# Optimization experiments

Hardware: AMD Instinct MI355X
Metric: run time of the kernel (lower is better)

Reference implementation:

```python
import jax, jax.numpy as jnp
import numpy as np

N = 10000        # nodes
F_IN = 128       # node features (data.num_node_features)
OUT = 16         # out_channels
H = 32           # attention heads
C1 = 4 * OUT     # hidden per-head dim (4*out_channels)
E = 80000        # directed edges
EPS = 1e-5       # BatchNorm eps
NEG = 0.2        # GATConv LeakyReLU negative_slope


def _gat(x, src, dst, W, a_s, a_d, b, n, C):
    # PyG GATConv, shared lin, concat=False (mean over heads)
    h = (x @ W).reshape(n, H, C)                    # [n,H,C]
    e_src = jnp.sum(h * a_s, -1)                    # [n,H] (alpha from x_j)
    e_dst = jnp.sum(h * a_d, -1)                    # [n,H] (alpha from x_i)
    e = jax.nn.leaky_relu(e_src[src] + e_dst[dst], NEG)     # [E',H]
    m = jax.ops.segment_max(e, dst, num_segments=n)         # segment softmax
    p = jnp.exp(e - m[dst])
    z = jax.ops.segment_sum(p, dst, num_segments=n)
    alpha = p / z[dst]
    out = jax.ops.segment_sum(alpha[:, :, None] * h[src], dst, num_segments=n)
    return out.mean(1) + b                          # mean over heads + bias


def _bn(x, g, b, m, v):  # eval-mode BatchNorm1d (running stats)
    return (x - m) * g / jnp.sqrt(v + EPS) + b


def setup_inputs():
    k = jax.random.split(jax.random.key(0), 40)
    rn = lambda i, s, sc=0.1: jax.random.normal(k[i], s, jnp.float32) * sc
    d = {"x": jax.random.normal(k[0], (N, F_IN), jnp.float32),
         "edge_index": jax.random.randint(k[1], (2, E), 0, N, jnp.int32)}
    # 4 GATConv layers
    d.update(W1=rn(2, (F_IN, H * C1)), as1=rn(3, (H, C1)), ad1=rn(4, (H, C1)), b1=rn(5, (C1,)))
    d.update(W2=rn(6, (C1, H * OUT)), as2=rn(7, (H, OUT)), ad2=rn(8, (H, OUT)), b2=rn(9, (OUT,)))
    d.update(W3=rn(10, (F_IN, H * C1)), as3=rn(11, (H, C1)), ad3=rn(12, (H, C1)), b3=rn(13, (C1,)))
    d.update(W4=rn(14, (C1, H * OUT)), as4=rn(15, (H, OUT)), ad4=rn(16, (H, OUT)), b4=rn(17, (OUT,)))
    # ResidualNetwork(1 block): 1x1 Conv1d over L=1 == matmul
    d.update(rwa=rn(18, (F_IN, OUT)), rba=rn(19, (OUT,)),
             bn1g=jnp.ones(OUT), bn1b=jnp.zeros(OUT), bn1m=rn(20, (OUT,)), bn1v=jnp.abs(rn(21, (OUT,))) + 1.0,
             rwb=rn(22, (OUT, OUT)), rbb=rn(23, (OUT,)),
             bn2g=jnp.ones(OUT), bn2b=jnp.zeros(OUT), bn2m=rn(24, (OUT,)), bn2v=jnp.abs(rn(25, (OUT,))) + 1.0,
             wsc=rn(26, (F_IN, OUT)), bsc=rn(27, (OUT,)),
             bnsg=jnp.ones(OUT), bnsb=jnp.zeros(OUT), bnsm=rn(28, (OUT,)), bnsv=jnp.abs(rn(29, (OUT,))) + 1.0,
             wfc=rn(30, (OUT, OUT)), bfc=rn(31, (OUT,)))
    return d


def reference(x, edge_index, W1, as1, ad1, b1, W2, as2, ad2, b2,
              W3, as3, ad3, b3, W4, as4, ad4, b4,
              rwa, rba, bn1g, bn1b, bn1m, bn1v, rwb, rbb, bn2g, bn2b, bn2m, bn2v,
              wsc, bsc, bnsg, bnsb, bnsm, bnsv, wfc, bfc):
    n = x.shape[0]
    loops = jnp.arange(n, dtype=edge_index.dtype)  # add_self_loops=True
    s2t_src = jnp.concatenate([edge_index[0], loops])  # flow source_to_target
    s2t_dst = jnp.concatenate([edge_index[1], loops])
    t2s_src = jnp.concatenate([edge_index[1], loops])  # flow target_to_source
    t2s_dst = jnp.concatenate([edge_index[0], loops])
    # dropout in original is unassigned (no-op); eval mode assumed
    x_s = jax.nn.elu(_gat(x, s2t_src, s2t_dst, W1, as1, ad1, b1, n, C1))
    x_in = jax.nn.elu(_gat(x_s, s2t_src, s2t_dst, W2, as2, ad2, b2, n, OUT))
    x_t = jax.nn.elu(_gat(x, t2s_src, t2s_dst, W3, as3, ad3, b3, n, C1))
    x_out = jax.nn.elu(_gat(x_t, t2s_src, t2s_dst, W4, as4, ad4, b4, n, OUT))
    # ResidualNetwork: block + identity avg-pool (L=1) + fc
    h = jax.nn.relu(_bn(x @ rwa + rba, bn1g, bn1b, bn1m, bn1v))
    h = _bn(h @ rwb + rbb, bn2g, bn2b, bn2m, bn2v)
    sc = _bn(x @ wsc + bsc, bnsg, bnsb, bnsm, bnsv)
    x_self = jax.nn.relu(h + sc) @ wfc + bfc
    return (x_in, x_out, x_self)
```

## Files before the change

kernel.cpp:

```cpp
#include <hip/hip_runtime.h>
#include <stdint.h>

__device__ __forceinline__ float bf2f(unsigned short u) {
  union { unsigned int i; float f; } v; v.i = ((unsigned int)u) << 16; return v.f;
}
__device__ __forceinline__ unsigned short f2bf(float f) {
  union { float f; unsigned int i; } v; v.f = f;
  unsigned int i = v.i;
  unsigned int r = (i + 0x7fffu + ((i >> 16) & 1u)) >> 16;
  return (unsigned short)r;
}

typedef __bf16 bf16x8 __attribute__((ext_vector_type(8)));
typedef float f32x4 __attribute__((ext_vector_type(4)));
union ABfrag { int4 i4; bf16x8 v; };

#if __has_builtin(__builtin_amdgcn_cvt_pk_fp8_f32) && __has_builtin(__builtin_amdgcn_cvt_pk_f32_fp8)
#define HW_FP8 1
#else
#define HW_FP8 0
#endif

__device__ __forceinline__ unsigned char f2fp8_sw(float f) {
  union { float f; unsigned int u; } v; v.f = f;
  unsigned int s = (v.u >> 24) & 0x80;
  float a = fabsf(f);
  if (a >= 448.f) return (unsigned char)(s | 0x7E);
  v.f = a;
  int ex = (int)(v.u >> 23);
  unsigned int man = v.u & 0x7FFFFFu;
  if (ex >= 121) {
    unsigned int val = ((unsigned int)(ex - 120) << 3) | (man >> 20);
    unsigned int rem = man & 0xFFFFFu;
    if (rem > 0x80000u || (rem == 0x80000u && (val & 1))) val++;
    if (val > 0x7E) val = 0x7E;
    return (unsigned char)(s | val);
  }
  int q = (int)(a * 512.f + 0.5f);
  if (q > 8) q = 8;
  return (unsigned char)(s | (unsigned int)q);
}
__device__ __forceinline__ float fp8dec_sw(unsigned char c) {
  unsigned int e = (c >> 3) & 15u, m = c & 7u;
  float v;
  if (e) { union { unsigned int u; float f; } x; x.u = ((e + 120) << 23) | (m << 20); v = x.f; }
  else v = (float)m * 0.001953125f;
  return (c & 0x80) ? -v : v;
}
__device__ __forceinline__ unsigned char f2fp8(float f) {
#if HW_FP8
  int v = __builtin_amdgcn_cvt_pk_fp8_f32(f, f, 0, false);
  return (unsigned char)(v & 0xFF);
#else
  return f2fp8_sw(f);
#endif
}
__device__ __forceinline__ void dec16(int4 g, float o[16]) {
#if HW_FP8
  { auto p = __builtin_amdgcn_cvt_pk_f32_fp8(g.x, false); o[0]=p[0]; o[1]=p[1]; }
  { auto p = __builtin_amdgcn_cvt_pk_f32_fp8(g.x, true ); o[2]=p[0]; o[3]=p[1]; }
  { auto p = __builtin_amdgcn_cvt_pk_f32_fp8(g.y, false); o[4]=p[0]; o[5]=p[1]; }
  { auto p = __builtin_amdgcn_cvt_pk_f32_fp8(g.y, true ); o[6]=p[0]; o[7]=p[1]; }
  { auto p = __builtin_amdgcn_cvt_pk_f32_fp8(g.z, false); o[8]=p[0]; o[9]=p[1]; }
  { auto p = __builtin_amdgcn_cvt_pk_f32_fp8(g.z, true ); o[10]=p[0]; o[11]=p[1]; }
  { auto p = __builtin_amdgcn_cvt_pk_f32_fp8(g.w, false); o[12]=p[0]; o[13]=p[1]; }
  { auto p = __builtin_amdgcn_cvt_pk_f32_fp8(g.w, true ); o[14]=p[0]; o[15]=p[1]; }
#else
  unsigned int w[4] = {(unsigned)g.x, (unsigned)g.y, (unsigned)g.z, (unsigned)g.w};
#pragma unroll
  for (int d = 0; d < 4; ++d)
#pragma unroll
    for (int b = 0; b < 4; ++b) o[d*4+b] = fp8dec_sw((unsigned char)((w[d] >> (b*8)) & 0xFF));
#endif
}

__device__ __forceinline__ float lrelu_clamp(float e) {
  e = (e > 0.f) ? e : 0.2f * e;
  return fminf(e, 80.f);
}

__global__ __launch_bounds__(256) void k_detect(const unsigned int* __restrict__ x, int* flag) {
  __shared__ int cnt;
  if (threadIdx.x == 0) cnt = 0;
  __syncthreads();
  int c = 0;
  for (int i = threadIdx.x; i < 1024; i += 256) {
    unsigned int lo = x[i] & 0xFFFFu;
    int ex = (int)((lo >> 7) & 0xFF);
    if (ex >= 100 && ex <= 140) c++;
  }
  atomicAdd(&cnt, c);
  __syncthreads();
  if (threadIdx.x == 0) flag[0] = (cnt > 600) ? 1 : 0;
}

struct PrepDesc {
  const void* csrc[32]; float* cdst[32]; int cn[32];
  const void* x; float* xc; unsigned short* xp;
  const void* W1; const void* W2; const void* W3; const void* W4;
  unsigned short* P1; unsigned short* P2; unsigned short* P3; unsigned short* P4;
  int* degAB;
  int nxb, xtotal, ctotal, ndeg2;
};
__global__ __launch_bounds__(256) void k_prep(PrepDesc d, const int* __restrict__ flag) {
  int isbf = *flag;
  int b = blockIdx.x;
  if (b < d.nxb) {
    int i = b * 256 + threadIdx.x;
    if (i < d.xtotal) {
      float v = isbf ? bf2f(((const unsigned short*)d.x)[i]) : ((const float*)d.x)[i];
      d.xc[i] = v;
      int row = i >> 7, c = i & 127;
      int tm = row >> 4, mr = row & 15;
      int s = c >> 5, quad = (c >> 3) & 3, j = c & 7;
      size_t idx = (((size_t)tm * 4 + s) * 64 + quad * 16 + mr) * 8 + j;
      d.xp[idx] = f2bf(v);
    }
    return;
  }
  b -= d.nxb;
  if (b < 288) {
    int u = b * 256 + threadIdx.x;
    const void* W; unsigned short* P; int K, N, lu;
    if (u < 32768)      { W = d.W1; P = d.P1; K = 128; N = 2048; lu = u; }
    else if (u < 36864) { W = d.W2; P = d.P2; K = 64;  N = 512;  lu = u - 32768; }
    else if (u < 69632) { W = d.W3; P = d.P3; K = 128; N = 2048; lu = u - 36864; }
    else                { W = d.W4; P = d.P4; K = 64;  N = 512;  lu = u - 69632; }
    int ksteps = K >> 5;
    int g = lu / (ksteps * 64);
    int rem = lu - g * (ksteps * 64);
    int s = rem >> 6, lane = rem & 63;
    int mr = lane & 15, quad = lane >> 4;
    int col = g * 16 + mr;
    int kbase = s * 32 + quad * 8;
#pragma unroll
    for (int j = 0; j < 8; ++j) {
      size_t src = (size_t)(kbase + j) * N + col;
      float v = isbf ? bf2f(((const unsigned short*)W)[src]) : ((const float*)W)[src];
      P[(size_t)lu * 8 + j] = f2bf(v);
    }
    return;
  }
  b -= 288;
  if (b < 4) {
    for (int idx = b * 256 + threadIdx.x; idx < d.ctotal; idx += 4 * 256) {
      int t = 0, off = idx;
      while (off >= d.cn[t]) { off -= d.cn[t]; ++t; }
      float v = isbf ? bf2f(((const unsigned short*)d.csrc[t])[off])
                     : ((const float*)d.csrc[t])[off];
      d.cdst[t][off] = v;
    }
    return;
  }
  b -= 4;
  for (int idx = b * 256 + threadIdx.x; idx < d.ndeg2; idx += 8 * 256) d.degAB[idx] = 0;
}

__global__ __launch_bounds__(256) void k_deg_count(const int* __restrict__ ei, int* degA, int* degB, int E) {
  int e = blockIdx.x * 256 + threadIdx.x;
  if (e < E) { atomicAdd(&degA[ei[E + e]], 1); atomicAdd(&degB[ei[e]], 1); }
}
__global__ __launch_bounds__(1024) void k_exscan2(const int* __restrict__ degA, const int* __restrict__ degB,
                                                  int* __restrict__ rowA, int* __restrict__ rowB,
                                                  int* __restrict__ colA, int* __restrict__ colB,
                                                  int* __restrict__ curA, int* __restrict__ curB, int n) {
  const int* deg = (blockIdx.x == 0) ? degA : degB;
  int* row = (blockIdx.x == 0) ? rowA : rowB;
  int* colx = (blockIdx.x == 0) ? colA : colB;
  int* curx = (blockIdx.x == 0) ? curA : curB;
  __shared__ int wsum[16], wbase[16];
  __shared__ int carry;
  if (threadIdx.x == 0) carry = 0;
  __syncthreads();
  int lane = threadIdx.x & 63, w = threadIdx.x >> 6;
  int chunks = (n + 1023) >> 10;
  for (int ch = 0; ch < chunks; ++ch) {
    int i = (ch << 10) + threadIdx.x;
    int v = (i < n) ? deg[i] : 0;
    int sc = v;
#pragma unroll
    for (int o = 1; o < 64; o <<= 1) { int t = __shfl_up(sc, o); if (lane >= o) sc += t; }
    if (lane == 63) wsum[w] = sc;
    __syncthreads();
    if (threadIdx.x < 16) {
      int v2 = wsum[threadIdx.x], s2 = v2;
#pragma unroll
      for (int o = 1; o < 16; o <<= 1) { int t = __shfl_up(s2, o); if (lane >= o) s2 += t; }
      wbase[threadIdx.x] = s2 - v2;
      if (threadIdx.x == 15) wsum[15] = s2;
    }
    __syncthreads();
    if (i < n) {
      int rv = carry + wbase[w] + (sc - v) + i;
      row[i] = rv;
      colx[rv] = i;
      curx[i] = rv + 1;
    }
    __syncthreads();
    if (threadIdx.x == 0) carry += wsum[15];
    __syncthreads();
  }
  if (threadIdx.x == 0) row[n] = carry + n;
}
__global__ __launch_bounds__(256) void k_scatter(const int* __restrict__ ei, int* colA, int* colB,
                                                 int* curA, int* curB, int E) {
  int e = blockIdx.x * 256 + threadIdx.x;
  if (e < E) {
    int s = ei[e], d = ei[E + e];
    colA[atomicAdd(&curA[d], 1)] = s;
    colB[atomicAdd(&curB[s], 1)] = d;
  }
}

union SMem {
  unsigned char tile[4][16][64];
  struct { float xs[16][128]; float ha[16][16]; float tt[16][16]; } res;
};

template<int CH, int KSTEPS>
__device__ __forceinline__ void mm_es_body(int vblk,
    const unsigned short* __restrict__ Ap, const unsigned short* __restrict__ Bp,
    unsigned char* __restrict__ C, const float* __restrict__ a_s, const float* __restrict__ a_d,
    float* __restrict__ es, float* __restrict__ ed, int N, SMem* sm) {
  int wid = threadIdx.x >> 6;
  int wg = vblk * 4 + wid;
  int ntiles = N >> 6;
  int tm = wg / ntiles, tn = wg % ntiles;
  int lane = threadIdx.x & 63;
  int mr = lane & 15, quad = lane >> 4;
  const unsigned short* ap = Ap + ((size_t)tm * KSTEPS) * 512 + lane * 8;
  const unsigned short* bp = Bp + ((size_t)tn * 4 * KSTEPS) * 512 + lane * 8;
  f32x4 acc[4];
#pragma unroll
  for (int i = 0; i < 4; i++) acc[i] = (f32x4){0.f, 0.f, 0.f, 0.f};
#pragma unroll
  for (int s = 0; s < KSTEPS; ++s) {
    ABfrag a; a.i4 = *(const int4*)(ap + s * 512);
#pragma unroll
    for (int nt = 0; nt < 4; ++nt) {
      ABfrag b; b.i4 = *(const int4*)(bp + (size_t)(nt * KSTEPS + s) * 512);
      acc[nt] = __builtin_amdgcn_mfma_f32_16x16x32_bf16(a.v, b.v, acc[nt], 0, 0, 0);
    }
  }
#pragma unroll
  for (int nt = 0; nt < 4; ++nt)
#pragma unroll
    for (int r = 0; r < 4; ++r)
      sm->tile[wid][quad * 4 + r][nt * 16 + mr] = f2fp8(acc[nt][r]);
  __syncthreads();
  {
    int r16 = lane >> 2, seg = lane & 3;
    int4 val = *(const int4*)&sm->tile[wid][r16][seg * 16];
    *(int4*)(C + (size_t)(tm * 16 + r16) * N + tn * 64 + seg * 16) = val;
  }
  if (CH == 64) {
    float pes[4] = {0.f,0.f,0.f,0.f}, ped[4] = {0.f,0.f,0.f,0.f};
    const float* asr = a_s + tn * 64;
    const float* adr = a_d + tn * 64;
#pragma unroll
    for (int nt = 0; nt < 4; ++nt) {
      float ws = asr[nt * 16 + mr], wd = adr[nt * 16 + mr];
#pragma unroll
      for (int r = 0; r < 4; ++r) { pes[r] += acc[nt][r] * ws; ped[r] += acc[nt][r] * wd; }
    }
#pragma unroll
    for (int m = 1; m < 16; m <<= 1)
#pragma unroll
      for (int r = 0; r < 4; ++r) {
        pes[r] += __shfl_xor(pes[r], m);
        ped[r] += __shfl_xor(ped[r], m);
      }
    if (mr == 0) {
#pragma unroll
      for (int r = 0; r < 4; ++r) {
        int row = tm * 16 + quad * 4 + r;
        es[row * 32 + tn] = pes[r];
        ed[row * 32 + tn] = ped[r];
      }
    }
  } else {
    float pes[4][4], ped[4][4];
#pragma unroll
    for (int nt = 0; nt < 4; ++nt) {
      float ws = a_s[(tn * 4 + nt) * 16 + mr];
      float wd = a_d[(tn * 4 + nt) * 16 + mr];
#pragma unroll
      for (int r = 0; r < 4; ++r) { pes[nt][r] = acc[nt][r] * ws; ped[nt][r] = acc[nt][r] * wd; }
    }
#pragma unroll
    for (int m = 1; m < 16; m <<= 1)
#pragma unroll
      for (int nt = 0; nt < 4; ++nt)
#pragma unroll
        for (int r = 0; r < 4; ++r) {
          pes[nt][r] += __shfl_xor(pes[nt][r], m);
          ped[nt][r] += __shfl_xor(ped[nt][r], m);
        }
    if (mr == 0) {
#pragma unroll
      for (int nt = 0; nt < 4; ++nt)
#pragma unroll
        for (int r = 0; r < 4; ++r) {
          int row = tm * 16 + quad * 4 + r;
          es[row * 32 + tn * 4 + nt] = pes[nt][r];
          ed[row * 32 + tn * 4 + nt] = ped[nt][r];
        }
    }
  }
}

struct MM13Desc {
  const unsigned short* Ap;
  const unsigned short* B1; const unsigned short* B3;
  unsigned char* C1; unsigned char* C3;
  const float* as1; const float* ad1; const float* as3; const float* ad3;
  float* es1; float* ed1; float* es3; float* ed3;
  int mmblks;
  const float* xc;
  const float* rp[20];
  void* outbase; size_t eoff; int n;
  const int* flag;
};
__global__ __launch_bounds__(256) void k_mm13res(MM13Desc d) {
  __shared__ SMem sm;
  int b = blockIdx.x;
  if (b < d.mmblks) {
    mm_es_body<64,4>(b, d.Ap, d.B1, d.C1, d.as1, d.ad1, d.es1, d.ed1, 2048, &sm);
    return;
  }
  b -= d.mmblks;
  if (b < d.mmblks) {
    mm_es_body<64,4>(b, d.Ap, d.B3, d.C3, d.as3, d.ad3, d.es3, d.ed3, 2048, &sm);
    return;
  }
  b -= d.mmblks;
  int nodebase = b * 16;
  for (int t = threadIdx.x; t < 16 * 128; t += 256)
    sm.res.xs[t >> 7][t & 127] = d.xc[(size_t)(nodebase + (t >> 7)) * 128 + (t & 127)];
  __syncthreads();
  int ni = threadIdx.x >> 4, c = threadIdx.x & 15;
  const float* rwa = d.rp[0]; const float* rba = d.rp[1];
  const float* bn1g = d.rp[2]; const float* bn1b = d.rp[3];
  const float* bn1m = d.rp[4]; const float* bn1v = d.rp[5];
  const float* rwb = d.rp[6]; const float* rbb = d.rp[7];
  const float* bn2g = d.rp[8]; const float* bn2b = d.rp[9];
  const float* bn2m = d.rp[10]; const float* bn2v = d.rp[11];
  const float* wsc = d.rp[12]; const float* bsc = d.rp[13];
  const float* bnsg = d.rp[14]; const float* bnsb = d.rp[15];
  const float* bnsm = d.rp[16]; const float* bnsv = d.rp[17];
  const float* wfc = d.rp[18]; const float* bfc = d.rp[19];
  float ya = 0.f, ysc = 0.f;
  for (int k = 0; k < 128; ++k) {
    float xv = sm.res.xs[ni][k];
    ya  += xv * rwa[k * 16 + c];
    ysc += xv * wsc[k * 16 + c];
  }
  ya += rba[c]; ysc += bsc[c];
  float s1 = bn1g[c] * rsqrtf(bn1v[c] + 1e-5f);
  ya = (ya - bn1m[c]) * s1 + bn1b[c];
  ya = fmaxf(ya, 0.f);
  float ss = bnsg[c] * rsqrtf(bnsv[c] + 1e-5f);
  ysc = (ysc - bnsm[c]) * ss + bnsb[c];
  sm.res.ha[ni][c] = ya;
  __syncthreads();
  float h2 = rbb[c];
  for (int k = 0; k < 16; ++k) h2 += sm.res.ha[ni][k] * rwb[k * 16 + c];
  float s2 = bn2g[c] * rsqrtf(bn2v[c] + 1e-5f);
  h2 = (h2 - bn2m[c]) * s2 + bn2b[c];
  sm.res.tt[ni][c] = fmaxf(h2 + ysc, 0.f);
  __syncthreads();
  float o = bfc[c];
  for (int k = 0; k < 16; ++k) o += sm.res.tt[ni][k] * wfc[k * 16 + c];
  size_t oo = d.eoff + (size_t)(nodebase + ni) * 16 + c;
  if (*d.flag) ((unsigned short*)d.outbase)[oo] = f2bf(o);
  else         ((float*)d.outbase)[oo] = o;
}

__global__ __launch_bounds__(256) void k_g64(const unsigned char* __restrict__ h1,
                                             const unsigned char* __restrict__ h3,
                                             const float* __restrict__ es1, const float* __restrict__ ed1,
                                             const float* __restrict__ es3, const float* __restrict__ ed3,
                                             const int* __restrict__ rowA, const int* __restrict__ colA,
                                             const int* __restrict__ rowB, const int* __restrict__ colB,
                                             const float* __restrict__ b1, const float* __restrict__ b3,
                                             unsigned short* __restrict__ xsp, unsigned short* __restrict__ xtp,
                                             int n, int gb) {
  int b = blockIdx.x;
  const unsigned char* h; const float *es, *ed, *bias; const int *rowp, *col; unsigned short* outp;
  if (b < gb) { h = h1; es = es1; ed = ed1; rowp = rowA; col = colA; bias = b1; outp = xsp; }
  else { b -= gb; h = h3; es = es3; ed = ed3; rowp = rowB; col = colB; bias = b3; outp = xtp; }
  int wid = threadIdx.x >> 6, lane = threadIdx.x & 63;
  int i = b * 4 + wid;
  if (i >= n) return;
  int hd0 = lane >> 2, hd1 = 16 + hd0;
  float e0 = ed[i * 32 + hd0];
  float e1 = ed[i * 32 + hd1];
  int beg = rowp[i], end = rowp[i + 1];
  int deg = end - beg;
  int colv = (lane < deg) ? col[beg + lane] : 0;
  float acc0[16], acc1[16];
#pragma unroll
  for (int k = 0; k < 16; ++k) { acc0[k] = 0.f; acc1[k] = 0.f; }
  float Z0 = 0.f, Z1 = 0.f;
  for (int j = 0; j < deg; ++j) {
    int s = (j < 64) ? __shfl(colv, j) : col[beg + j];
    const int4* hp = (const int4*)(h + (size_t)s * 2048);
    int4 g0 = hp[lane];
    int4 g1 = hp[64 + lane];
    float q0 = __expf(lrelu_clamp(es[s * 32 + hd0] + e0));
    float q1 = __expf(lrelu_clamp(es[s * 32 + hd1] + e1));
    Z0 += q0; Z1 += q1;
    float d0[16], d1[16];
    dec16(g0, d0); dec16(g1, d1);
#pragma unroll
    for (int k = 0; k < 16; ++k) { acc0[k] += q0 * d0[k]; acc1[k] += q1 * d1[k]; }
  }
  float zi0 = 1.0f / Z0, zi1 = 1.0f / Z1;
  float v[16];
#pragma unroll
  for (int k = 0; k < 16; ++k) v[k] = acc0[k] * zi0 + acc1[k] * zi1;
#pragma unroll
  for (int m = 4; m < 64; m <<= 1)
#pragma unroll
    for (int k = 0; k < 16; ++k) v[k] += __shfl_xor(v[k], m);
  if (lane < 4) {
    int tm = i >> 4, mr = i & 15;
    unsigned short ob[16];
#pragma unroll
    for (int k = 0; k < 16; ++k) {
      float t = v[k] * (1.f / 32.f) + bias[lane * 16 + k];
      t = (t > 0.f) ? t : (__expf(t) - 1.f);
      ob[k] = f2bf(t);
    }
    int s0 = lane >> 1;
#pragma unroll
    for (int g2 = 0; g2 < 2; ++g2) {
      size_t idx = (((size_t)tm * 2 + s0) * 64 + ((lane & 1) * 2 + g2) * 16 + mr) * 8;
      *(int4*)(outp + idx) = *(const int4*)(ob + g2 * 8);
    }
  }
}

__global__ __launch_bounds__(256) void k_mm24(const unsigned short* __restrict__ xsp,
                                              const unsigned short* __restrict__ xtp,
                                              const unsigned short* __restrict__ W2p,
                                              const unsigned short* __restrict__ W4p,
                                              unsigned char* __restrict__ h2, unsigned char* __restrict__ h4,
                                              const float* __restrict__ as2, const float* __restrict__ ad2,
                                              const float* __restrict__ as4, const float* __restrict__ ad4,
                                              float* __restrict__ es2, float* __restrict__ ed2,
                                              float* __restrict__ es4, float* __restrict__ ed4,
                                              int mmblks) {
  __shared__ SMem sm;
  int b = blockIdx.x;
  if (b < mmblks)
    mm_es_body<16,2>(b, xsp, W2p, h2, as2, ad2, es2, ed2, 512, &sm);
  else
    mm_es_body<16,2>(b - mmblks, xtp, W4p, h4, as4, ad4, es4, ed4, 512, &sm);
}

__global__ __launch_bounds__(256) void k_g16(const unsigned char* __restrict__ h2,
                                             const unsigned char* __restrict__ h4,
                                             const float* __restrict__ es2, const float* __restrict__ ed2,
                                             const float* __restrict__ es4, const float* __restrict__ ed4,
                                             const int* __restrict__ rowA, const int* __restrict__ colA,
                                             const int* __restrict__ rowB, const int* __restrict__ colB,
                                             const float* __restrict__ b2, const float* __restrict__ b4,
                                             void* __restrict__ outbase, int n, int gb,
                                             const int* __restrict__ flag) {
  int b = blockIdx.x;
  const unsigned char* h; const float *es, *ed, *bias; const int *rowp, *col; size_t eoff;
  if (b < gb) { h = h2; es = es2; ed = ed2; rowp = rowA; col = colA; bias = b2; eoff = 0; }
  else { b -= gb; h = h4; es = es4; ed = ed4; rowp = rowB; col = colB; bias = b4; eoff = (size_t)n * 16; }
  int wid = threadIdx.x >> 6, lane = threadIdx.x & 63;
  int i = b * 4 + wid;
  if (i >= n) return;
  int hh = lane & 31, j2 = lane >> 5;
  float ev = ed[i * 32 + hh];
  int beg = rowp[i], end = rowp[i + 1];
  int deg = end - beg;
  int colv = (lane < deg) ? col[beg + lane] : 0;
  float acc[16];
#pragma unroll
  for (int k = 0; k < 16; ++k) acc[k] = 0.f;
  float Z = 0.f;
  for (int j = j2; j < deg; j += 2) {
    int s = (j < 64) ? __shfl(colv, j) : col[beg + j];
    int4 g = ((const int4*)(h + (size_t)s * 512))[hh];
    float q = __expf(lrelu_clamp(es[s * 32 + hh] + ev));
    Z += q;
    float d[16];
    dec16(g, d);
#pragma unroll
    for (int k = 0; k < 16; ++k) acc[k] += q * d[k];
  }
  Z += __shfl_xor(Z, 32);
  float zi = 1.0f / Z;
  float v[16];
#pragma unroll
  for (int k = 0; k < 16; ++k) v[k] = acc[k] * zi;
#pragma unroll
  for (int m = 1; m < 64; m <<= 1)
#pragma unroll
    for (int k = 0; k < 16; ++k) v[k] += __shfl_xor(v[k], m);
  if (lane == 0) {
    int isbf = *flag;
    if (isbf) {
      unsigned short ob[16];
#pragma unroll
      for (int k = 0; k < 16; ++k) {
        float t = v[k] * (1.f / 32.f) + bias[k];
        t = (t > 0.f) ? t : (__expf(t) - 1.f);
        ob[k] = f2bf(t);
      }
      unsigned short* o = (unsigned short*)outbase + eoff + (size_t)i * 16;
      *(int4*)o = *(const int4*)ob;
      *(int4*)(o + 8) = *(const int4*)(ob + 8);
    } else {
      float* o = (float*)outbase + eoff + (size_t)i * 16;
#pragma unroll
      for (int k = 0; k < 16; ++k) {
        float t = v[k] * (1.f / 32.f) + bias[k];
        t = (t > 0.f) ? t : (__expf(t) - 1.f);
        o[k] = t;
      }
    }
  }
}

extern "C" void kernel_launch(void* const* d_in, const int* in_sizes, int n_in,
                              void* d_out, int out_size, void* d_ws, size_t ws_size,
                              hipStream_t stream) {
  const int n = in_sizes[0] / 128;
  const int E = in_sizes[1] / 2;
  const int* ei = (const int*)d_in[1];

  char* wsp = (char*)d_ws; size_t off = 0;
  auto alloc = [&](size_t bytes) -> void* {
    void* p = wsp + off; off = (off + bytes + 255) & ~(size_t)255; return p;
  };
  int* flag = (int*)alloc(4);
  float* xc = (float*)alloc((size_t)n * 128 * 4);
  unsigned short* xp = (unsigned short*)alloc((size_t)n * 128 * 2);
  unsigned short* W1p = (unsigned short*)alloc((size_t)2048 * 128 * 2);
  unsigned short* W2p = (unsigned short*)alloc((size_t)512 * 64 * 2);
  unsigned short* W3p = (unsigned short*)alloc((size_t)2048 * 128 * 2);
  unsigned short* W4p = (unsigned short*)alloc((size_t)512 * 64 * 2);
  unsigned char* h1 = (unsigned char*)alloc((size_t)n * 2048);
  unsigned char* h3 = (unsigned char*)alloc((size_t)n * 2048);
  unsigned char* h2 = (unsigned char*)alloc((size_t)n * 512);
  unsigned char* h4 = (unsigned char*)alloc((size_t)n * 512);
  float* es1 = (float*)alloc((size_t)n * 32 * 4);
  float* ed1 = (float*)alloc((size_t)n * 32 * 4);
  float* es3 = (float*)alloc((size_t)n * 32 * 4);
  float* ed3 = (float*)alloc((size_t)n * 32 * 4);
  float* es2 = (float*)alloc((size_t)n * 32 * 4);
  float* ed2 = (float*)alloc((size_t)n * 32 * 4);
  float* es4 = (float*)alloc((size_t)n * 32 * 4);
  float* ed4 = (float*)alloc((size_t)n * 32 * 4);
  unsigned short* xsp = (unsigned short*)alloc((size_t)n * 64 * 2);
  unsigned short* xtp = (unsigned short*)alloc((size_t)n * 64 * 2);
  int* rowA = (int*)alloc((size_t)(n + 1) * 4);
  int* rowB = (int*)alloc((size_t)(n + 1) * 4);
  int* colA = (int*)alloc((size_t)(E + n) * 4);
  int* colB = (int*)alloc((size_t)(E + n) * 4);
  int* degAB = (int*)alloc((size_t)2 * n * 4);
  int* degA = degAB, * degB = degAB + n;
  int* curA = (int*)alloc((size_t)n * 4);
  int* curB = (int*)alloc((size_t)n * 4);

  static const int cidx[32] = {3,4,5, 7,8,9, 11,12,13, 15,16,17,
                               18,19,20,21,22,23,24,25,26,27,28,29,
                               30,31,32,33,34,35,36,37};
  PrepDesc pd;
  float* canon[38] = {nullptr};
  pd.ctotal = 0;
  for (int t = 0; t < 32; ++t) {
    int ii = cidx[t];
    canon[ii] = (float*)alloc((size_t)in_sizes[ii] * 4);
    pd.csrc[t] = d_in[ii];
    pd.cdst[t] = canon[ii];
    pd.cn[t] = in_sizes[ii];
    pd.ctotal += in_sizes[ii];
  }
  pd.x = d_in[0]; pd.xc = xc; pd.xp = xp;
  pd.W1 = d_in[2]; pd.W2 = d_in[6]; pd.W3 = d_in[10]; pd.W4 = d_in[14];
  pd.P1 = W1p; pd.P2 = W2p; pd.P3 = W3p; pd.P4 = W4p;
  pd.degAB = degAB;
  pd.nxb = (n * 128 + 255) / 256;
  pd.xtotal = n * 128;
  pd.ndeg2 = 2 * n;
  (void)ws_size; (void)n_in; (void)out_size;

  k_detect<<<1, 256, 0, stream>>>((const unsigned int*)d_in[0], flag);
  k_prep<<<pd.nxb + 288 + 4 + 8, 256, 0, stream>>>(pd, flag);

  k_deg_count<<<(E + 255) / 256, 256, 0, stream>>>(ei, degA, degB, E);
  k_exscan2<<<2, 1024, 0, stream>>>(degA, degB, rowA, rowB, colA, colB, curA, curB, n);
  k_scatter<<<(E + 255) / 256, 256, 0, stream>>>(ei, colA, colB, curA, curB, E);

  const int mt = n / 16;
  const int mmblks64 = mt * 32 / 4;
  const int mmblks16 = mt * 8 / 4;
  const int gb = (n + 3) / 4;

  MM13Desc md;
  md.Ap = xp; md.B1 = W1p; md.B3 = W3p; md.C1 = h1; md.C3 = h3;
  md.as1 = canon[3]; md.ad1 = canon[4]; md.as3 = canon[11]; md.ad3 = canon[12];
  md.es1 = es1; md.ed1 = ed1; md.es3 = es3; md.ed3 = ed3;
  md.mmblks = mmblks64;
  md.xc = xc;
  for (int t = 0; t < 20; ++t) md.rp[t] = canon[18 + t];
  md.outbase = d_out; md.eoff = (size_t)2 * n * 16; md.n = n; md.flag = flag;
  k_mm13res<<<2 * mmblks64 + n / 16, 256, 0, stream>>>(md);

  k_g64<<<2 * gb, 256, 0, stream>>>(h1, h3, es1, ed1, es3, ed3,
                                    rowA, colA, rowB, colB,
                                    canon[5], canon[13], xsp, xtp, n, gb);
  k_mm24<<<2 * mmblks16, 256, 0, stream>>>(xsp, xtp, W2p, W4p, h2, h4,
                                           canon[7], canon[8], canon[15], canon[16],
                                           es2, ed2, es4, ed4, mmblks16);
  k_g16<<<2 * gb, 256, 0, stream>>>(h2, h4, es2, ed2, es4, ed4,
                                    rowA, colA, rowB, colB,
                                    canon[9], canon[17], d_out, n, gb, flag);
}
```

Before: 323.8 us.

## Fold dtype detection and degree counting into prep kernel; parallelize CSR scan

Removes the separate detect and degree-count launches. Every prep block now recomputes the bf16/fp32 detection itself, and the edge degree atomics run as extra blocks of k_prep, with the degree buffers zeroed by a memset beforehand. The exclusive scan becomes a two-pass chunked scan, one wave per 1024-element chunk, replacing the serial loop over chunks with block-wide syncs. This saves launches and scan serialization, at the cost of each prep block redundantly reading 4KB of x and adding a memset call.

```diff
diff --git a/kernel.cpp b/kernel.cpp
--- a/kernel.cpp
+++ b/kernel.cpp
@@ -79,40 +79,39 @@
   return fminf(e, 80.f);
 }
 
-__global__ __launch_bounds__(256) void k_detect(const unsigned int* __restrict__ x, int* flag) {
-  __shared__ int cnt;
-  if (threadIdx.x == 0) cnt = 0;
-  __syncthreads();
-  int c = 0;
-  for (int i = threadIdx.x; i < 1024; i += 256) {
-    unsigned int lo = x[i] & 0xFFFFu;
-    int ex = (int)((lo >> 7) & 0xFF);
-    if (ex >= 100 && ex <= 140) c++;
-  }
-  atomicAdd(&cnt, c);
-  __syncthreads();
-  if (threadIdx.x == 0) flag[0] = (cnt > 600) ? 1 : 0;
-}
-
 struct PrepDesc {
   const void* csrc[32]; float* cdst[32]; int cn[32];
   const void* x; float* xc; unsigned short* xp;
   const void* W1; const void* W2; const void* W3; const void* W4;
   unsigned short* P1; unsigned short* P2; unsigned short* P3; unsigned short* P4;
-  int* degAB;
-  int nxb, xtotal, ctotal, ndeg2;
+  const int* ei; int* degA; int* degB; int E;
+  int* flagout;
+  int nxb, xtotal, ctotal, ndgb;
 };
-__global__ __launch_bounds__(256) void k_prep(PrepDesc d, const int* __restrict__ flag) {
-  int isbf = *flag;
+__global__ __launch_bounds__(256) void k_prep(PrepDesc d) {
+  int c = 0;
+  for (int i = threadIdx.x; i < 1024; i += 256) {
+    unsigned int lo = ((const unsigned int*)d.x)[i] & 0xFFFFu;
+    int ex = (int)((lo >> 7) & 0xFF);
+    if (ex >= 100 && ex <= 140) c++;
+  }
+#pragma unroll
+  for (int m = 1; m < 64; m <<= 1) c += __shfl_xor(c, m);
+  __shared__ int redc[4];
+  if ((threadIdx.x & 63) == 0) redc[threadIdx.x >> 6] = c;
+  __syncthreads();
+  int isbf = (redc[0] + redc[1] + redc[2] + redc[3]) > 600;
+  if (blockIdx.x == 0 && threadIdx.x == 0) d.flagout[0] = isbf;
+
   int b = blockIdx.x;
   if (b < d.nxb) {
     int i = b * 256 + threadIdx.x;
     if (i < d.xtotal) {
       float v = isbf ? bf2f(((const unsigned short*)d.x)[i]) : ((const float*)d.x)[i];
       d.xc[i] = v;
-      int row = i >> 7, c = i & 127;
+      int row = i >> 7, cc = i & 127;
       int tm = row >> 4, mr = row & 15;
-      int s = c >> 5, quad = (c >> 3) & 3, j = c & 7;
+      int s = cc >> 5, quad = (cc >> 3) & 3, j = cc & 7;
       size_t idx = (((size_t)tm * 4 + s) * 64 + quad * 16 + mr) * 8 + j;
       d.xp[idx] = f2bf(v);
     }
@@ -153,13 +152,13 @@
     return;
   }
   b -= 4;
-  for (int idx = b * 256 + threadIdx.x; idx < d.ndeg2; idx += 8 * 256) d.degAB[idx] = 0;
-}
-
-__global__ __launch_bounds__(256) void k_deg_count(const int* __restrict__ ei, int* degA, int* degB, int E) {
-  int e = blockIdx.x * 256 + threadIdx.x;
-  if (e < E) { atomicAdd(&degA[ei[E + e]], 1); atomicAdd(&degB[ei[e]], 1); }
-}
+  int e = b * 256 + threadIdx.x;
+  if (e < d.E) {
+    atomicAdd(&d.degA[d.ei[d.E + e]], 1);
+    atomicAdd(&d.degB[d.ei[e]], 1);
+  }
+}
+
 __global__ __launch_bounds__(1024) void k_exscan2(const int* __restrict__ degA, const int* __restrict__ degB,
                                                   int* __restrict__ rowA, int* __restrict__ rowB,
                                                   int* __restrict__ colA, int* __restrict__ colB,
@@ -168,39 +167,45 @@
   int* row = (blockIdx.x == 0) ? rowA : rowB;
   int* colx = (blockIdx.x == 0) ? colA : colB;
   int* curx = (blockIdx.x == 0) ? curA : curB;
-  __shared__ int wsum[16], wbase[16];
-  __shared__ int carry;
-  if (threadIdx.x == 0) carry = 0;
+  __shared__ int csum[16], cbase[16];
+  int lane = threadIdx.x & 63, w = threadIdx.x >> 6;
+  int nch = (n + 1023) >> 10;
+  if (w < nch) {
+    int base = w << 10;
+    int s = 0;
+    for (int t = lane; t < 1024; t += 64) {
+      int i = base + t;
+      s += (i < n) ? deg[i] : 0;
+    }
+#pragma unroll
+    for (int m = 1; m < 64; m <<= 1) s += __shfl_xor(s, m);
+    if (lane == 0) csum[w] = s;
+  }
   __syncthreads();
-  int lane = threadIdx.x & 63, w = threadIdx.x >> 6;
-  int chunks = (n + 1023) >> 10;
-  for (int ch = 0; ch < chunks; ++ch) {
-    int i = (ch << 10) + threadIdx.x;
-    int v = (i < n) ? deg[i] : 0;
-    int sc = v;
-#pragma unroll
-    for (int o = 1; o < 64; o <<= 1) { int t = __shfl_up(sc, o); if (lane >= o) sc += t; }
-    if (lane == 63) wsum[w] = sc;
-    __syncthreads();
-    if (threadIdx.x < 16) {
-      int v2 = wsum[threadIdx.x], s2 = v2;
-#pragma unroll
-      for (int o = 1; o < 16; o <<= 1) { int t = __shfl_up(s2, o); if (lane >= o) s2 += t; }
-      wbase[threadIdx.x] = s2 - v2;
-      if (threadIdx.x == 15) wsum[15] = s2;
-    }
-    __syncthreads();
-    if (i < n) {
-      int rv = carry + wbase[w] + (sc - v) + i;
-      row[i] = rv;
-      colx[rv] = i;
-      curx[i] = rv + 1;
-    }
-    __syncthreads();
-    if (threadIdx.x == 0) carry += wsum[15];
-    __syncthreads();
-  }
-  if (threadIdx.x == 0) row[n] = carry + n;
+  if (threadIdx.x == 0) {
+    int run = 0;
+    for (int c2 = 0; c2 < nch; ++c2) { cbase[c2] = run; run += csum[c2]; }
+    row[n] = run + n;
+  }
+  __syncthreads();
+  if (w < nch) {
+    int base = w << 10;
+    int run = cbase[w];
+    for (int t0 = 0; t0 < 1024; t0 += 64) {
+      int i = base + t0 + lane;
+      int v = (i < n) ? deg[i] : 0;
+      int sc = v;
+#pragma unroll
+      for (int o = 1; o < 64; o <<= 1) { int t = __shfl_up(sc, o); if (lane >= o) sc += t; }
+      if (i < n) {
+        int rv = run + (sc - v) + i;
+        row[i] = rv;
+        colx[rv] = i;
+        curx[i] = rv + 1;
+      }
+      run += __shfl(sc, 63);
+    }
+  }
 }
 __global__ __launch_bounds__(256) void k_scatter(const int* __restrict__ ei, int* colA, int* colB,
                                                  int* curA, int* curB, int E) {
@@ -432,10 +437,10 @@
       t = (t > 0.f) ? t : (__expf(t) - 1.f);
       ob[k] = f2bf(t);
     }
-    int s0 = lane >> 1;
+    int s0w = lane >> 1;
 #pragma unroll
     for (int g2 = 0; g2 < 2; ++g2) {
-      size_t idx = (((size_t)tm * 2 + s0) * 64 + ((lane & 1) * 2 + g2) * 16 + mr) * 8;
+      size_t idx = (((size_t)tm * 2 + s0w) * 64 + ((lane & 1) * 2 + g2) * 16 + mr) * 8;
       *(int4*)(outp + idx) = *(const int4*)(ob + g2 * 8);
     }
   }
@@ -586,16 +591,16 @@
   pd.x = d_in[0]; pd.xc = xc; pd.xp = xp;
   pd.W1 = d_in[2]; pd.W2 = d_in[6]; pd.W3 = d_in[10]; pd.W4 = d_in[14];
   pd.P1 = W1p; pd.P2 = W2p; pd.P3 = W3p; pd.P4 = W4p;
-  pd.degAB = degAB;
+  pd.ei = ei; pd.degA = degA; pd.degB = degB; pd.E = E;
+  pd.flagout = flag;
   pd.nxb = (n * 128 + 255) / 256;
   pd.xtotal = n * 128;
-  pd.ndeg2 = 2 * n;
+  pd.ndgb = (E + 255) / 256;
   (void)ws_size; (void)n_in; (void)out_size;
 
-  k_detect<<<1, 256, 0, stream>>>((const unsigned int*)d_in[0], flag);
-  k_prep<<<pd.nxb + 288 + 4 + 8, 256, 0, stream>>>(pd, flag);
-
-  k_deg_count<<<(E + 255) / 256, 256, 0, stream>>>(ei, degA, degB, E);
+  hipMemsetAsync(degAB, 0, (size_t)2 * n * 4, stream);
+  k_prep<<<pd.nxb + 288 + 4 + pd.ndgb, 256, 0, stream>>>(pd);
+
   k_exscan2<<<2, 1024, 0, stream>>>(degA, degB, rowA, rowB, colA, colB, curA, curB, n);
   k_scatter<<<(E + 255) / 256, 256, 0, stream>>>(ei, colA, colB, curA, curB, E);
 
```

New measurement: 325.8 us. Within noise of the previous version (+0.6%).
